# Performance work log

Hardware: AMD Instinct MI355X
Metric: run time of the kernel (lower is better)

## Reference

```python
import jax, jax.numpy as jnp
import numpy as np
import math

B, C, H, W = 32, 3, 512, 512
K = 16
OUT_H, OUT_W = 512, 512

def _ctrl_pts(k):
    gs = int(math.sqrt(k))
    lin = jnp.linspace(-1.0, 1.0, gs)
    gy, gx = jnp.meshgrid(lin, lin, indexing='ij')
    return jnp.stack([gx, gy], axis=-1).reshape(-1, 2)

def setup_inputs() -> dict:
    key = jax.random.key(0)
    k1, k2, k3, k4 = jax.random.split(key, 4)
    x = jax.random.normal(k1, (B, C, H, W), jnp.float32)
    conv_w = jax.random.normal(k2, (8, C, 7, 7), jnp.float32) * 0.05
    conv_b = jax.random.normal(k3, (8,), jnp.float32) * 0.05
    fc_w = jax.random.normal(k4, (2 * K, 8), jnp.float32) * 0.01
    fc_b = jnp.asarray(_ctrl_pts(K).reshape(-1))  # module inits bias to ctrl grid
    return {"x": x, "conv_w": conv_w, "conv_b": conv_b, "fc_w": fc_w, "fc_b": fc_b}

def _U(sq):
    # U(r) = r^2 * log(r^2 + 1e-6), expressed with squared distance sq = r^2
    return sq * jnp.log(sq + 1e-6)

def _tps_grid(src, tgt, out_h, out_w):
    # src: [K,2] shared across batch (fixed ctrl grid), tgt: [B,K,2]
    Bb, Kk, _ = tgt.shape
    lin_y = jnp.linspace(-1.0, 1.0, out_h)
    lin_x = jnp.linspace(-1.0, 1.0, out_w)
    gy, gx = jnp.meshgrid(lin_y, lin_x, indexing='ij')
    grid = jnp.stack([gx, gy], axis=-1).reshape(-1, 2)  # [N,2]
    N = out_h * out_w
    # RBF kernel between output grid and source ctrl pts: [N,K]
    d2 = jnp.sum((grid[:, None, :] - src[None, :, :]) ** 2, axis=-1)
    U = _U(d2)
    # TPS system matrix L [K+3,K+3]; src is batch-shared so build it once
    src_d2 = jnp.sum((src[:, None, :] - src[None, :, :]) ** 2, axis=-1)
    P = jnp.concatenate([jnp.ones((Kk, 1)), src], axis=1)  # [K,3]
    L = jnp.zeros((Kk + 3, Kk + 3))
    L = L.at[:Kk, :Kk].set(_U(src_d2))
    L = L.at[:Kk, Kk:].set(P)
    L = L.at[Kk:, :Kk].set(P.T)
    Y = jnp.concatenate([tgt, jnp.zeros((Bb, 3, 2))], axis=1)  # [B,K+3,2]
    Wmat = jnp.linalg.solve(L[None], Y)  # [B,K+3,2]
    Pg = jnp.concatenate([jnp.ones((N, 1)), grid], axis=1)  # [N,3]
    mapped = (jnp.einsum('nk,bkc->bnc', U, Wmat[:, :Kk])
              + jnp.einsum('np,bpc->bnc', Pg, Wmat[:, Kk:]))
    return mapped.reshape(Bb, out_h, out_w, 2)

def _grid_sample(x, grid):
    # bilinear, zero padding, align_corners=False (torch defaults)
    Bb, Cc, Hh, Ww = x.shape
    ix = ((grid[..., 0] + 1.0) * Ww - 1.0) * 0.5
    iy = ((grid[..., 1] + 1.0) * Hh - 1.0) * 0.5
    x0 = jnp.floor(ix)
    y0 = jnp.floor(iy)
    wx1 = ix - x0
    wy1 = iy - y0
    x0i = x0.astype(jnp.int32)
    y0i = y0.astype(jnp.int32)

    def gather(img, yy, xx):
        valid = ((yy >= 0) & (yy < Hh) & (xx >= 0) & (xx < Ww)).astype(img.dtype)
        yc = jnp.clip(yy, 0, Hh - 1)
        xc = jnp.clip(xx, 0, Ww - 1)
        return img[:, yc, xc] * valid[None]

    def per(img, x0i, y0i, wx1, wy1):
        wx0 = 1.0 - wx1
        wy0 = 1.0 - wy1
        v00 = gather(img, y0i, x0i)
        v01 = gather(img, y0i, x0i + 1)
        v10 = gather(img, y0i + 1, x0i)
        v11 = gather(img, y0i + 1, x0i + 1)
        return (v00 * (wy0 * wx0)[None] + v01 * (wy0 * wx1)[None]
                + v10 * (wy1 * wx0)[None] + v11 * (wy1 * wx1)[None])

    return jax.vmap(per)(x, x0i, y0i, wx1, wy1)

def reference(x, conv_w, conv_b, fc_w, fc_b):
    # localization: conv7x7 -> relu -> global avg pool -> fc
    feat = jax.lax.conv_general_dilated(
        x, conv_w, window_strides=(1, 1), padding='VALID',
        dimension_numbers=('NCHW', 'OIHW', 'NCHW'))
    feat = jax.nn.relu(feat + conv_b[None, :, None, None])
    pooled = feat.mean(axis=(2, 3))  # [B,8] (AdaptiveAvgPool2d(1))
    pred = (pooled @ fc_w.T + fc_b).reshape(-1, K, 2)  # [B,K,2]
    src = _ctrl_pts(K)
    grid = _tps_grid(src, pred, OUT_H, OUT_W)  # [B,OUT_H,OUT_W,2]
    return _grid_sample(x, grid)
```

## Files before the change

### kernel.cpp

```cpp
#include <hip/hip_runtime.h>
#include <hip/hip_bf16.h>
#include <hip/hip_fp16.h>
#include <math.h>

#define BATCH 32
#define CH_IN 3
#define CH_OUT 8
#define IMG 512
#define KSZ 7
#define CONV_OUT 506
#define KPTS 16
#define TILES_PER_B 64

#define SROWS 23
#define ROW_PX 264
#define ROW_U4 33
#define ROW_BYTES 528
#define SMEM_DW (CH_IN * SROWS * (ROW_BYTES / 4))
#define NCHUNK (CH_IN * SROWS * ROW_U4)

#define BPB 8

typedef _Float16 half8_t __attribute__((ext_vector_type(8)));
typedef float f32x4_t __attribute__((ext_vector_type(4)));

__device__ __forceinline__ unsigned short f2h_bits(float f) {
    _Float16 h = (_Float16)f;
    unsigned short u;
    __builtin_memcpy(&u, &h, 2);
    return u;
}
__device__ __forceinline__ float h2f_bits(unsigned short u) {
    _Float16 h;
    __builtin_memcpy(&h, &u, 2);
    return (float)h;
}
__device__ __forceinline__ unsigned int pk2(float a, float b) {
    return (unsigned int)f2h_bits(a) | ((unsigned int)f2h_bits(b) << 16);
}

__global__ void wprep_kernel(const float* __restrict__ w, uint4* __restrict__ afrag) {
    int idx = blockIdx.x * 256 + threadIdx.x;
    if (idx >= 6 * 64) return;
    int s = idx >> 6, l = idx & 63;
    int m = l & 15;
    int dlt = m >> 3, o = m & 7;
    int oct = s * 4 + (l >> 4);
    int c = oct >> 3, ky = oct & 7;
    unsigned short h[8];
    #pragma unroll
    for (int j = 0; j < 8; ++j) {
        int kx = j - dlt;
        float v = 0.f;
        if (ky < KSZ && kx >= 0 && kx < KSZ)
            v = w[((o * CH_IN + c) * KSZ + ky) * KSZ + kx];
        h[j] = f2h_bits(v);
    }
    uint4 out;
    __builtin_memcpy(&out, h, 16);
    afrag[idx] = out;
}

template <bool FUSED>
__global__ __launch_bounds__(256)
void conv_pool_kernel(const float* __restrict__ x, unsigned short* __restrict__ xh,
                      const uint4* __restrict__ afrag, const float* __restrict__ conv_b,
                      float* __restrict__ partial) {
    __shared__ unsigned int smem[SMEM_DW];
    __shared__ float red[4][8];

    int blk = blockIdx.x;
    int b = blk >> 6;
    int rem0 = blk & 63;
    int stripe = rem0 >> 1;
    int half = rem0 & 1;
    int ybase = stripe * 16;
    int x0 = half * 256;
    int tid = threadIdx.x;

    {
        const float* xb = x + (size_t)b * CH_IN * IMG * IMG;
        unsigned short* xhb = xh + (size_t)b * CH_IN * IMG * IMG;
        for (int idx4 = tid; idx4 < NCHUNK; idx4 += 256) {
            int c = idx4 / (SROWS * ROW_U4);
            int rem = idx4 - c * (SROWS * ROW_U4);
            int r = rem / ROW_U4;
            int u4 = rem - r * ROW_U4;
            int grow = ybase + r;
            int gcol = x0 + (u4 << 3);
            uint4 v = make_uint4(0u, 0u, 0u, 0u);
            if (grow < IMG && gcol < IMG) {
                const float* rp = xb + ((size_t)c * IMG + grow) * IMG + gcol;
                float4 f0 = *(const float4*)rp;
                float4 f1 = *(const float4*)(rp + 4);
                v.x = pk2(f0.x, f0.y);
                v.y = pk2(f0.z, f0.w);
                v.z = pk2(f1.x, f1.y);
                v.w = pk2(f1.z, f1.w);
            }
            *(uint4*)((char*)smem + (c * SROWS + r) * ROW_BYTES + (u4 << 4)) = v;
            if (FUSED && r < 16 && u4 < 32)
                *(uint4*)(xhb + ((size_t)c * IMG + grow) * IMG + gcol) = v;
        }
    }
    __syncthreads();

    int l = tid & 63, w = tid >> 6;
    int n = l & 15, g = l >> 4;

    uint4 at[6];
    #pragma unroll
    for (int s = 0; s < 6; ++s) at[s] = afrag[s * 64 + l];

    int rowb[6];
    #pragma unroll
    for (int s = 0; s < 6; ++s) {
        int oct = s * 4 + g;
        int c = oct >> 3, ky = oct & 7;
        rowb[s] = (c * SROWS + n + ky) * ROW_BYTES + w * 64;
    }

    float bias_[4];
    {
        int ob = (g & 1) * 4;
        #pragma unroll
        for (int r2 = 0; r2 < 4; ++r2) bias_[r2] = conv_b[ob + r2];
    }
    bool rowok = (ybase + n) < CONV_OUT;
    int dlt = g >> 1;
    float sums[4] = {0.f, 0.f, 0.f, 0.f};
    const char* sb = (const char*)smem;

    #pragma unroll
    for (int cc = 0; cc < 2; ++cc) {
        int off = cc * 256;
        #pragma unroll
        for (int u = 0; u < 4; ++u) {
            f32x4_t acc[4];
            #pragma unroll
            for (int d = 0; d < 4; ++d) acc[d] = (f32x4_t){0.f, 0.f, 0.f, 0.f};

            #pragma unroll
            for (int s = 0; s < 6; ++s) {
                uint4 lo = *(const uint4*)(sb + rowb[s] + off + (u << 4));
                uint4 hi = *(const uint4*)(sb + rowb[s] + off + (u << 4) + 16);
                unsigned int eu[8] = {lo.x, lo.y, lo.z, lo.w, hi.x, hi.y, hi.z, hi.w};
                half8_t a;
                __builtin_memcpy(&a, &at[s], 16);
                #pragma unroll
                for (int d = 0; d < 4; ++d) {
                    uint4 bu = make_uint4(eu[d], eu[d + 1], eu[d + 2], eu[d + 3]);
                    half8_t bf;
                    __builtin_memcpy(&bf, &bu, 16);
                    acc[d] = __builtin_amdgcn_mfma_f32_16x16x32_f16(a, bf, acc[d], 0, 0, 0);
                }
            }

            #pragma unroll
            for (int d = 0; d < 4; ++d) {
                int col = x0 + cc * 128 + 32 * w + 8 * u + 2 * d + dlt;
                bool colok = col < CONV_OUT;
                #pragma unroll
                for (int r2 = 0; r2 < 4; ++r2) {
                    float v = acc[d][r2] + bias_[r2];
                    v = v > 0.f ? v : 0.f;
                    sums[r2] += (rowok && colok) ? v : 0.f;
                }
            }
        }
    }

    #pragma unroll
    for (int r2 = 0; r2 < 4; ++r2) {
        sums[r2] += __shfl_xor(sums[r2], 1, 64);
        sums[r2] += __shfl_xor(sums[r2], 2, 64);
        sums[r2] += __shfl_xor(sums[r2], 4, 64);
        sums[r2] += __shfl_xor(sums[r2], 8, 64);
        sums[r2] += __shfl_xor(sums[r2], 32, 64);
    }
    if (l == 0) {
        #pragma unroll
        for (int r2 = 0; r2 < 4; ++r2) red[w][r2] = sums[r2];
    }
    if (l == 16) {
        #pragma unroll
        for (int r2 = 0; r2 < 4; ++r2) red[w][4 + r2] = sums[r2];
    }
    __syncthreads();
    if (tid < CH_OUT) {
        float s = red[0][tid] + red[1][tid] + red[2][tid] + red[3][tid];
        partial[tid * (BATCH * TILES_PER_B) + b * TILES_PER_B + stripe * 2 + half] = s;
    }
}

__device__ __forceinline__ double ctrl_lin(int i) { return -1.0 + (2.0 / 3.0) * i; }

__global__ void solve_kernel(const float* __restrict__ partial,
                             const float* __restrict__ fc_w,
                             const float* __restrict__ fc_b,
                             float* __restrict__ Wf) {
    __shared__ double L[19][19];
    __shared__ double Ys[19][64];
    __shared__ double piv_fac[19];
    __shared__ int piv_idx;
    __shared__ float pooledS[BATCH][CH_OUT];

    int t = threadIdx.x;

    for (int p = t; p < BATCH * CH_OUT; p += 64) {
        int b = p >> 3, o = p & 7;
        const float4* pp = (const float4*)(partial + o * (BATCH * TILES_PER_B) + b * TILES_PER_B);
        double a0 = 0.0, a1 = 0.0, a2 = 0.0, a3 = 0.0;
        #pragma unroll
        for (int gq = 0; gq < TILES_PER_B / 4; ++gq) {
            float4 v = pp[gq];
            a0 += (double)v.x; a1 += (double)v.y;
            a2 += (double)v.z; a3 += (double)v.w;
        }
        pooledS[b][o] = (float)(((a0 + a1) + (a2 + a3)) / ((double)CONV_OUT * (double)CONV_OUT));
    }
    __syncthreads();

    {
        int b = t >> 1, c = t & 1;
        for (int k = 0; k < KPTS; ++k) {
            int j = k * 2 + c;
            double s = (double)fc_b[j];
            for (int o = 0; o < CH_OUT; ++o)
                s += (double)pooledS[b][o] * (double)fc_w[j * CH_OUT + o];
            Ys[k][t] = s;
        }
        for (int k = KPTS; k < 19; ++k) Ys[k][t] = 0.0;
    }

    for (int p = t; p < 19 * 19; p += 64) {
        int r = p / 19, cc = p % 19;
        double v;
        if (r < KPTS && cc < KPTS) {
            double dx = ctrl_lin(r & 3) - ctrl_lin(cc & 3);
            double dy = ctrl_lin(r >> 2) - ctrl_lin(cc >> 2);
            double d2 = dx * dx + dy * dy;
            v = d2 * log(d2 + 1e-6);
        } else if (r < KPTS) {
            v = (cc == KPTS) ? 1.0 : (cc == KPTS + 1 ? ctrl_lin(r & 3) : ctrl_lin(r >> 2));
        } else if (cc < KPTS) {
            v = (r == KPTS) ? 1.0 : (r == KPTS + 1 ? ctrl_lin(cc & 3) : ctrl_lin(cc >> 2));
        } else v = 0.0;
        L[r][cc] = v;
    }
    __syncthreads();

    for (int k = 0; k < 19; ++k) {
        if (t == 0) {
            int pi = k; double mx = fabs(L[k][k]);
            for (int i = k + 1; i < 19; ++i) {
                double a = fabs(L[i][k]);
                if (a > mx) { mx = a; pi = i; }
            }
            piv_idx = pi;
        }
        __syncthreads();
        int pi = piv_idx;
        if (pi != k) {
            if (t < 19) { double tmp = L[k][t]; L[k][t] = L[pi][t]; L[pi][t] = tmp; }
            { double tmp = Ys[k][t]; Ys[k][t] = Ys[pi][t]; Ys[pi][t] = tmp; }
        }
        __syncthreads();
        if (t > k && t < 19) piv_fac[t] = L[t][k] / L[k][k];
        __syncthreads();
        if (t > k && t < 19) {
            double lkj = L[k][t];
            for (int i = k + 1; i < 19; ++i) L[i][t] -= piv_fac[i] * lkj;
        }
        {
            double ykt = Ys[k][t];
            for (int i = k + 1; i < 19; ++i) Ys[i][t] -= piv_fac[i] * ykt;
        }
        __syncthreads();
    }

    for (int k = 18; k >= 0; --k) {
        double s = Ys[k][t];
        for (int j = k + 1; j < 19; ++j) s -= L[k][j] * Ys[j][t];
        Ys[k][t] = s / L[k][k];
    }

    {
        int b = t >> 1, c = t & 1;
        for (int k = 0; k < 19; ++k)
            Wf[(b * 19 + k) * 2 + c] = (float)Ys[k][t];
    }
}

template <bool H16>
__global__ __launch_bounds__(256)
void tps_sample_kernel(const float* __restrict__ x, const unsigned short* __restrict__ xh,
                       const float* __restrict__ Wf, float* __restrict__ out) {
    int blk = blockIdx.x;
    int bgrp = blk >> 10;
    int pix = ((blk & 1023) << 8) | threadIdx.x;
    int i = pix >> 9, j = pix & 511;

    float gx = -1.f + (2.f / 511.f) * (float)j;
    float gy = -1.f + (2.f / 511.f) * (float)i;

    float U[KPTS];
    #pragma unroll
    for (int k = 0; k < KPTS; ++k) {
        float sx = -1.f + (2.f / 3.f) * (float)(k & 3);
        float sy = -1.f + (2.f / 3.f) * (float)(k >> 2);
        float dx = gx - sx, dy = gy - sy;
        float d2 = dx * dx + dy * dy;
        U[k] = d2 * (0.69314718055994531f * __log2f(d2 + 1e-6f));
    }

    for (int b = bgrp * BPB; b < bgrp * BPB + BPB; ++b) {
        const float* Wb = Wf + b * 38;

        float mx = Wb[32] + gx * Wb[34] + gy * Wb[36];
        float my = Wb[33] + gx * Wb[35] + gy * Wb[37];
        #pragma unroll
        for (int k = 0; k < KPTS; ++k) {
            mx += U[k] * Wb[2 * k];
            my += U[k] * Wb[2 * k + 1];
        }

        float ix = (mx + 1.f) * 256.f - 0.5f;
        float iy = (my + 1.f) * 256.f - 0.5f;
        float x0f = floorf(ix), y0f = floorf(iy);
        int x0 = (int)x0f, y0 = (int)y0f;
        int x1 = x0 + 1, y1 = y0 + 1;
        float wx1 = ix - x0f, wy1 = iy - y0f;
        float wx0 = 1.f - wx1, wy0 = 1.f - wy1;

        bool vx0 = (x0 >= 0) & (x0 < IMG), vx1 = (x1 >= 0) & (x1 < IMG);
        bool vy0 = (y0 >= 0) & (y0 < IMG), vy1 = (y1 >= 0) & (y1 < IMG);
        int xc0 = min(max(x0, 0), IMG - 1), xc1 = min(max(x1, 0), IMG - 1);
        int yc0 = min(max(y0, 0), IMG - 1), yc1 = min(max(y1, 0), IMG - 1);

        float w00 = (vy0 && vx0) ? wy0 * wx0 : 0.f;
        float w01 = (vy0 && vx1) ? wy0 * wx1 : 0.f;
        float w10 = (vy1 && vx0) ? wy1 * wx0 : 0.f;
        float w11 = (vy1 && vx1) ? wy1 * wx1 : 0.f;

        int o00 = yc0 * IMG + xc0, o01 = yc0 * IMG + xc1;
        int o10 = yc1 * IMG + xc0, o11 = yc1 * IMG + xc1;

        #pragma unroll
        for (int c = 0; c < CH_IN; ++c) {
            float v;
            if (H16) {
                const unsigned short* xp = xh + ((size_t)b * CH_IN + c) * IMG * IMG;
                v = h2f_bits(xp[o00]) * w00 + h2f_bits(xp[o01]) * w01
                  + h2f_bits(xp[o10]) * w10 + h2f_bits(xp[o11]) * w11;
            } else {
                const float* xp = x + ((size_t)b * CH_IN + c) * IMG * IMG;
                v = xp[o00] * w00 + xp[o01] * w01 + xp[o10] * w10 + xp[o11] * w11;
            }
            out[(((size_t)b * CH_IN + c) << 18) + (i << 9) + j] = v;
        }
    }
}

extern "C" void kernel_launch(void* const* d_in, const int* in_sizes, int n_in,
                              void* d_out, int out_size, void* d_ws, size_t ws_size,
                              hipStream_t stream) {
    const float* x      = (const float*)d_in[0];
    const float* conv_w = (const float*)d_in[1];
    const float* conv_b = (const float*)d_in[2];
    const float* fc_w   = (const float*)d_in[3];
    const float* fc_b   = (const float*)d_in[4];
    float* out = (float*)d_out;

    char* ws = (char*)d_ws;
    uint4* afrag   = (uint4*)ws;
    float* partial = (float*)(ws + 8192);
    float* Wf      = (float*)(ws + 139264);
    unsigned short* xh = (unsigned short*)(ws + 147456);
    const size_t need = 147456 + (size_t)BATCH * CH_IN * IMG * IMG * 2;
    bool fused = ws_size >= need;

    wprep_kernel<<<dim3(2), dim3(256), 0, stream>>>(conv_w, afrag);
    if (fused) {
        conv_pool_kernel<true><<<dim3(BATCH * TILES_PER_B), dim3(256), 0, stream>>>(
            x, xh, afrag, conv_b, partial);
    } else {
        conv_pool_kernel<false><<<dim3(BATCH * TILES_PER_B), dim3(256), 0, stream>>>(
            x, xh, afrag, conv_b, partial);
    }
    solve_kernel<<<dim3(1), dim3(64), 0, stream>>>(partial, fc_w, fc_b, Wf);
    if (fused) {
        tps_sample_kernel<true><<<dim3(4 * 1024), dim3(256), 0, stream>>>(x, xh, Wf, out);
    } else {
        tps_sample_kernel<false><<<dim3(4 * 1024), dim3(256), 0, stream>>>(x, xh, Wf, out);
    }
}
```

Measured before the change: 141.4 us.

## Fuse weight prep and TPS solve into conv kernel via last-block atomic

Removes the separate weight-fragment prep kernel and the single-block solve kernel. Every conv block now builds the fp16 weight fragments in shared memory, and the last block to finish (found with an atomic counter after a threadfence) runs the pooled reduction, FC and 19x19 Gaussian elimination, reusing the conv shared memory. This cuts two launches and their serialisation gaps. In exchange it adds a memset launch, redundant weight prep in each of 2048 blocks, and a serial tail that depends on the last block.

```diff
diff --git a/kernel.cpp b/kernel.cpp
--- a/kernel.cpp
+++ b/kernel.cpp
@@ -13,7 +13,6 @@
 #define TILES_PER_B 64
 
 #define SROWS 23
-#define ROW_PX 264
 #define ROW_U4 33
 #define ROW_BYTES 528
 #define SMEM_DW (CH_IN * SROWS * (ROW_BYTES / 4))
@@ -38,36 +37,20 @@
 __device__ __forceinline__ unsigned int pk2(float a, float b) {
     return (unsigned int)f2h_bits(a) | ((unsigned int)f2h_bits(b) << 16);
 }
-
-__global__ void wprep_kernel(const float* __restrict__ w, uint4* __restrict__ afrag) {
-    int idx = blockIdx.x * 256 + threadIdx.x;
-    if (idx >= 6 * 64) return;
-    int s = idx >> 6, l = idx & 63;
-    int m = l & 15;
-    int dlt = m >> 3, o = m & 7;
-    int oct = s * 4 + (l >> 4);
-    int c = oct >> 3, ky = oct & 7;
-    unsigned short h[8];
-    #pragma unroll
-    for (int j = 0; j < 8; ++j) {
-        int kx = j - dlt;
-        float v = 0.f;
-        if (ky < KSZ && kx >= 0 && kx < KSZ)
-            v = w[((o * CH_IN + c) * KSZ + ky) * KSZ + kx];
-        h[j] = f2h_bits(v);
-    }
-    uint4 out;
-    __builtin_memcpy(&out, h, 16);
-    afrag[idx] = out;
-}
+__device__ __forceinline__ double ctrl_lin(int i) { return -1.0 + (2.0 / 3.0) * i; }
 
 template <bool FUSED>
 __global__ __launch_bounds__(256)
-void conv_pool_kernel(const float* __restrict__ x, unsigned short* __restrict__ xh,
-                      const uint4* __restrict__ afrag, const float* __restrict__ conv_b,
-                      float* __restrict__ partial) {
-    __shared__ unsigned int smem[SMEM_DW];
+void conv_mega_kernel(const float* __restrict__ x, unsigned short* __restrict__ xh,
+                      const float* __restrict__ conv_w, const float* __restrict__ conv_b,
+                      const float* __restrict__ fc_w, const float* __restrict__ fc_b,
+                      float* __restrict__ partial, float* __restrict__ Wf,
+                      unsigned int* __restrict__ counter) {
+    __shared__ __attribute__((aligned(16))) unsigned int smem[SMEM_DW];
+    __shared__ uint4 afrag_s[6 * 64];
     __shared__ float red[4][8];
+    __shared__ int lastflag;
+    __shared__ int piv_idx;
 
     int blk = blockIdx.x;
     int b = blk >> 6;
@@ -77,6 +60,26 @@
     int ybase = stripe * 16;
     int x0 = half * 256;
     int tid = threadIdx.x;
+
+    for (int idx = tid; idx < 6 * 64; idx += 256) {
+        int s = idx >> 6, l = idx & 63;
+        int m = l & 15;
+        int dlt = m >> 3, o = m & 7;
+        int oct = s * 4 + (l >> 4);
+        int c = oct >> 3, ky = oct & 7;
+        unsigned short h[8];
+        #pragma unroll
+        for (int j = 0; j < 8; ++j) {
+            int kx = j - dlt;
+            float v = 0.f;
+            if (ky < KSZ && kx >= 0 && kx < KSZ)
+                v = conv_w[((o * CH_IN + c) * KSZ + ky) * KSZ + kx];
+            h[j] = f2h_bits(v);
+        }
+        uint4 outv;
+        __builtin_memcpy(&outv, h, 16);
+        afrag_s[idx] = outv;
+    }
 
     {
         const float* xb = x + (size_t)b * CH_IN * IMG * IMG;
@@ -110,7 +113,7 @@
 
     uint4 at[6];
     #pragma unroll
-    for (int s = 0; s < 6; ++s) at[s] = afrag[s * 64 + l];
+    for (int s = 0; s < 6; ++s) at[s] = afrag_s[s * 64 + l];
 
     int rowb[6];
     #pragma unroll
@@ -191,25 +194,26 @@
         float s = red[0][tid] + red[1][tid] + red[2][tid] + red[3][tid];
         partial[tid * (BATCH * TILES_PER_B) + b * TILES_PER_B + stripe * 2 + half] = s;
     }
-}
-
-__device__ __forceinline__ double ctrl_lin(int i) { return -1.0 + (2.0 / 3.0) * i; }
-
-__global__ void solve_kernel(const float* __restrict__ partial,
-                             const float* __restrict__ fc_w,
-                             const float* __restrict__ fc_b,
-                             float* __restrict__ Wf) {
-    __shared__ double L[19][19];
-    __shared__ double Ys[19][64];
-    __shared__ double piv_fac[19];
-    __shared__ int piv_idx;
-    __shared__ float pooledS[BATCH][CH_OUT];
-
-    int t = threadIdx.x;
-
-    for (int p = t; p < BATCH * CH_OUT; p += 64) {
-        int b = p >> 3, o = p & 7;
-        const float4* pp = (const float4*)(partial + o * (BATCH * TILES_PER_B) + b * TILES_PER_B);
+
+    __threadfence();
+    __syncthreads();
+    if (tid == 0) {
+        unsigned int done = atomicAdd(counter, 1u);
+        lastflag = (done == gridDim.x - 1) ? 1 : 0;
+    }
+    __syncthreads();
+    if (!lastflag) return;
+    __threadfence();
+
+    double* L   = (double*)smem;
+    double* Ys  = L + 19 * 19;
+    double* piv = Ys + 19 * 64;
+    float* pooledS = (float*)(piv + 19);
+    int t = tid;
+
+    if (t < BATCH * CH_OUT) {
+        int bb = t >> 3, o = t & 7;
+        const float4* pp = (const float4*)(partial + o * (BATCH * TILES_PER_B) + bb * TILES_PER_B);
         double a0 = 0.0, a1 = 0.0, a2 = 0.0, a3 = 0.0;
         #pragma unroll
         for (int gq = 0; gq < TILES_PER_B / 4; ++gq) {
@@ -217,23 +221,24 @@
             a0 += (double)v.x; a1 += (double)v.y;
             a2 += (double)v.z; a3 += (double)v.w;
         }
-        pooledS[b][o] = (float)(((a0 + a1) + (a2 + a3)) / ((double)CONV_OUT * (double)CONV_OUT));
-    }
-    __syncthreads();
-
-    {
-        int b = t >> 1, c = t & 1;
+        pooledS[bb * CH_OUT + o] =
+            (float)(((a0 + a1) + (a2 + a3)) / ((double)CONV_OUT * (double)CONV_OUT));
+    }
+    __syncthreads();
+
+    if (t < 64) {
+        int bb = t >> 1, c = t & 1;
         for (int k = 0; k < KPTS; ++k) {
             int j = k * 2 + c;
             double s = (double)fc_b[j];
             for (int o = 0; o < CH_OUT; ++o)
-                s += (double)pooledS[b][o] * (double)fc_w[j * CH_OUT + o];
-            Ys[k][t] = s;
-        }
-        for (int k = KPTS; k < 19; ++k) Ys[k][t] = 0.0;
-    }
-
-    for (int p = t; p < 19 * 19; p += 64) {
+                s += (double)pooledS[bb * CH_OUT + o] * (double)fc_w[j * CH_OUT + o];
+            Ys[k * 64 + t] = s;
+        }
+        for (int k = KPTS; k < 19; ++k) Ys[k * 64 + t] = 0.0;
+    }
+
+    for (int p = t; p < 19 * 19; p += 256) {
         int r = p / 19, cc = p % 19;
         double v;
         if (r < KPTS && cc < KPTS) {
@@ -246,15 +251,15 @@
         } else if (cc < KPTS) {
             v = (r == KPTS) ? 1.0 : (r == KPTS + 1 ? ctrl_lin(cc & 3) : ctrl_lin(cc >> 2));
         } else v = 0.0;
-        L[r][cc] = v;
+        L[r * 19 + cc] = v;
     }
     __syncthreads();
 
     for (int k = 0; k < 19; ++k) {
         if (t == 0) {
-            int pi = k; double mx = fabs(L[k][k]);
+            int pi = k; double mx = fabs(L[k * 19 + k]);
             for (int i = k + 1; i < 19; ++i) {
-                double a = fabs(L[i][k]);
+                double a = fabs(L[i * 19 + k]);
                 if (a > mx) { mx = a; pi = i; }
             }
             piv_idx = pi;
@@ -262,33 +267,32 @@
         __syncthreads();
         int pi = piv_idx;
         if (pi != k) {
-            if (t < 19) { double tmp = L[k][t]; L[k][t] = L[pi][t]; L[pi][t] = tmp; }
-            { double tmp = Ys[k][t]; Ys[k][t] = Ys[pi][t]; Ys[pi][t] = tmp; }
+            if (t < 19) { double tmp = L[k * 19 + t]; L[k * 19 + t] = L[pi * 19 + t]; L[pi * 19 + t] = tmp; }
+            if (t < 64) { double tmp = Ys[k * 64 + t]; Ys[k * 64 + t] = Ys[pi * 64 + t]; Ys[pi * 64 + t] = tmp; }
         }
         __syncthreads();
-        if (t > k && t < 19) piv_fac[t] = L[t][k] / L[k][k];
+        if (t > k && t < 19) piv[t] = L[t * 19 + k] / L[k * 19 + k];
         __syncthreads();
         if (t > k && t < 19) {
-            double lkj = L[k][t];
-            for (int i = k + 1; i < 19; ++i) L[i][t] -= piv_fac[i] * lkj;
-        }
-        {
-            double ykt = Ys[k][t];
-            for (int i = k + 1; i < 19; ++i) Ys[i][t] -= piv_fac[i] * ykt;
+            double lkj = L[k * 19 + t];
+            for (int i = k + 1; i < 19; ++i) L[i * 19 + t] -= piv[i] * lkj;
+        }
+        if (t < 64) {
+            double ykt = Ys[k * 64 + t];
+            for (int i = k + 1; i < 19; ++i) Ys[i * 64 + t] -= piv[i] * ykt;
         }
         __syncthreads();
     }
 
-    for (int k = 18; k >= 0; --k) {
-        double s = Ys[k][t];
-        for (int j = k + 1; j < 19; ++j) s -= L[k][j] * Ys[j][t];
-        Ys[k][t] = s / L[k][k];
-    }
-
-    {
-        int b = t >> 1, c = t & 1;
+    if (t < 64) {
+        for (int k = 18; k >= 0; --k) {
+            double s = Ys[k * 64 + t];
+            for (int j = k + 1; j < 19; ++j) s -= L[k * 19 + j] * Ys[j * 64 + t];
+            Ys[k * 64 + t] = s / L[k * 19 + k];
+        }
+        int bb = t >> 1, c = t & 1;
         for (int k = 0; k < 19; ++k)
-            Wf[(b * 19 + k) * 2 + c] = (float)Ys[k][t];
+            Wf[(bb * 19 + k) * 2 + c] = (float)Ys[k * 64 + t];
     }
 }
 
@@ -373,25 +377,21 @@
     float* out = (float*)d_out;
 
     char* ws = (char*)d_ws;
-    uint4* afrag   = (uint4*)ws;
+    unsigned int* counter = (unsigned int*)ws;
     float* partial = (float*)(ws + 8192);
     float* Wf      = (float*)(ws + 139264);
     unsigned short* xh = (unsigned short*)(ws + 147456);
     const size_t need = 147456 + (size_t)BATCH * CH_IN * IMG * IMG * 2;
     bool fused = ws_size >= need;
 
-    wprep_kernel<<<dim3(2), dim3(256), 0, stream>>>(conv_w, afrag);
+    hipMemsetAsync(counter, 0, 64, stream);
     if (fused) {
-        conv_pool_kernel<true><<<dim3(BATCH * TILES_PER_B), dim3(256), 0, stream>>>(
-            x, xh, afrag, conv_b, partial);
-    } else {
-        conv_pool_kernel<false><<<dim3(BATCH * TILES_PER_B), dim3(256), 0, stream>>>(
-            x, xh, afrag, conv_b, partial);
-    }
-    solve_kernel<<<dim3(1), dim3(64), 0, stream>>>(partial, fc_w, fc_b, Wf);
-    if (fused) {
+        conv_mega_kernel<true><<<dim3(BATCH * TILES_PER_B), dim3(256), 0, stream>>>(
+            x, xh, conv_w, conv_b, fc_w, fc_b, partial, Wf, counter);
         tps_sample_kernel<true><<<dim3(4 * 1024), dim3(256), 0, stream>>>(x, xh, Wf, out);
     } else {
+        conv_mega_kernel<false><<<dim3(BATCH * TILES_PER_B), dim3(256), 0, stream>>>(
+            x, xh, conv_w, conv_b, fc_w, fc_b, partial, Wf, counter);
         tps_sample_kernel<false><<<dim3(4 * 1024), dim3(256), 0, stream>>>(x, xh, Wf, out);
     }
 }
```

Result: slower. 276.4 us (+95.4%).
